# Optimization experiments

Measured on AMD Instinct MI355X. Metric: run time of the kernel, lower is better.

Reference implementation:

```python
import jax, jax.numpy as jnp
import numpy as np

NUM_HEADS = 8
HEAD_SIZE = 64
INPUT = 512
OUT = NUM_HEADS * HEAD_SIZE
B, S = 4, 2048


def setup_inputs() -> dict:
    key = jax.random.key(0)
    ks = jax.random.split(key, 6)
    return {
        "key": jax.random.normal(ks[0], (B, S, INPUT), dtype=jnp.float32),
        "key_mask": jnp.zeros((B, 1, 1, S), dtype=jnp.float32),
        "query": jax.random.normal(ks[1], (B, S, INPUT), dtype=jnp.float32),
        "value": jax.random.normal(ks[2], (B, S, INPUT), dtype=jnp.float32),
        "wq": jax.random.normal(ks[3], (INPUT, OUT), dtype=jnp.float32) * (INPUT ** -0.5),
        "wk": jax.random.normal(ks[4], (INPUT, OUT), dtype=jnp.float32) * (INPUT ** -0.5),
        "wv": jax.random.normal(ks[5], (INPUT, OUT), dtype=jnp.float32) * (INPUT ** -0.5),
    }


def _split_heads(x):
    # [B, S, H*hd] -> [B, H, S, hd]
    b, s, _ = x.shape
    return x.reshape(b, s, NUM_HEADS, HEAD_SIZE).transpose(0, 2, 1, 3)


def reference(key, key_mask, query, value, wq, wk, wv):
    q = _split_heads(query @ wq)   # [B,H,S,hd]
    k = _split_heads(key @ wk)
    v = _split_heads(value @ wv)
    scale = 1.0 / jnp.sqrt(jnp.asarray(HEAD_SIZE, q.dtype))
    logits = jnp.einsum('bhqd,bhkd->bhqk', q, k) * scale + key_mask
    attn = jax.nn.softmax(logits, axis=-1)
    out = jnp.einsum('bhqk,bhkd->bhqd', attn, v)  # [B,H,S,hd]
    out = out.transpose(0, 2, 1, 3).reshape(out.shape[0], out.shape[2], OUT)
    return out
```

## Files before the change

kernel.cpp:

```cpp
#include <hip/hip_runtime.h>

typedef _Float16 f16;
typedef f16 f16x8 __attribute__((ext_vector_type(8)));
typedef f16 f16x4 __attribute__((ext_vector_type(4)));
typedef f16 f16x2 __attribute__((ext_vector_type(2)));
typedef float f32x4 __attribute__((ext_vector_type(4)));
typedef unsigned int u32;

#define MFMA16(a, b, c) __builtin_amdgcn_mfma_f32_16x16x32_f16(a, b, c, 0, 0, 0)

#define BATCH 4
#define NHEADS 8
#define HDIM 64
#define SEQ 2048
#define DIN 512
#define DOUT 512
#define LOG2E 1.44269504f
#define C1 0.18033688f

__device__ __forceinline__ void gl_lds16(const void* g, const void* l) {
  __builtin_amdgcn_global_load_lds(
      (const __attribute__((address_space(1))) u32*)g,
      (__attribute__((address_space(3))) u32*)l, 16, 0, 0);
}

__device__ __forceinline__ float fexp2(float x) {
  float r;
  asm("v_exp_f32 %0, %1" : "=v"(r) : "v"(x));
  return r;
}

__device__ __forceinline__ f16x2 pk2(float a, float b) {
  return __builtin_bit_cast(f16x2, __builtin_amdgcn_cvt_pkrtz(a, b));
}

__device__ __forceinline__ f16x4 pk4(float a, float b, float c, float d) {
  f16x2 u0 = pk2(a, b), u1 = pk2(c, d);
  f16x4 r;
  r[0] = u0[0]; r[1] = u0[1]; r[2] = u1[0]; r[3] = u1[1];
  return r;
}

__global__ __launch_bounds__(256) void prep_w(
    const float* __restrict__ wq, const float* __restrict__ wk,
    const float* __restrict__ wv, f16* __restrict__ wT) {
  __shared__ float tile[64][65];
  const float* w = blockIdx.z == 0 ? wq : (blockIdx.z == 1 ? wk : wv);
  f16* out = wT + (size_t)blockIdx.z * DIN * DOUT;
  int k0 = blockIdx.x * 64, n0 = blockIdx.y * 64;
  int t = threadIdx.x;
  int c = t & 63, rb = t >> 6;
#pragma unroll
  for (int ph = 0; ph < 16; ++ph) {
    int r = ph * 4 + rb;
    tile[r][c] = w[(size_t)(k0 + r) * DOUT + n0 + c];
  }
  __syncthreads();
#pragma unroll
  for (int ph = 0; ph < 16; ++ph) {
    int n = ph * 4 + rb;
    out[(size_t)(n0 + n) * DIN + k0 + c] = (f16)tile[c][n];
  }
}

__global__ __launch_bounds__(256, 3) void qkv_gemm(
    const float* __restrict__ xq, const float* __restrict__ xk,
    const float* __restrict__ xv, const f16* __restrict__ wT,
    f16* __restrict__ Qo, f16* __restrict__ Ko, f16* __restrict__ Vt) {
  __shared__ __attribute__((aligned(16))) f16 smem[16384];
  f16* As = smem;
  f16* Bs = smem + 8192;
  f16* CT = smem;

  int gemm = blockIdx.z;
  const float* x = gemm == 0 ? xq : (gemm == 1 ? xk : xv);
  const f16* wt = wT + (size_t)gemm * DIN * DOUT;
  int bx = blockIdx.x;
  int m0 = (bx & 63) * 128, n0 = (bx >> 6) * 128;
  int t = threadIdx.x, w = t >> 6, lane = t & 63;
  int lr = lane & 15, lq = lane >> 4;
  int wm = (w >> 1) * 64, wn = (w & 1) * 64;

  int tr = t >> 4, tc = t & 15;
  const float* xg = x + (size_t)(m0 + tr) * DIN + tc * 4;
  int aw[8];
#pragma unroll
  for (int ph = 0; ph < 8; ++ph) {
    int r = tr + 16 * ph;
    int phys = (tc >> 1) ^ (r & 7);
    aw[ph] = r * 64 + phys * 8 + (tc & 1) * 4;
  }

  int srow = lane >> 3;
  int schunk = (lane & 7) ^ srow;
  const f16* gb[4];
  const f16* lbb[4];
#pragma unroll
  for (int j = 0; j < 4; ++j) {
    int br = w * 32 + j * 8;
    gb[j] = wt + (size_t)(n0 + br + srow) * DIN + schunk * 8;
    lbb[j] = &Bs[__builtin_amdgcn_readfirstlane(br * 64)];
  }
  int xo0 = ((0 * 4 + lq) ^ (lr & 7)) * 8;
  int xo1 = ((1 * 4 + lq) ^ (lr & 7)) * 8;

  f32x4 zero = {0.f, 0.f, 0.f, 0.f};
  f32x4 acc[4][4];
#pragma unroll
  for (int i = 0; i < 4; ++i)
#pragma unroll
    for (int j = 0; j < 4; ++j) acc[i][j] = zero;

  for (int k0 = 0; k0 < DIN; k0 += 64) {
    __syncthreads();
#pragma unroll
    for (int j = 0; j < 4; ++j) gl_lds16(gb[j] + k0, lbb[j]);
#pragma unroll
    for (int ph = 0; ph < 8; ++ph) {
      float4 a = *(const float4*)(xg + (size_t)ph * 16 * DIN + k0);
      *(f16x4*)&As[aw[ph]] = pk4(a.x, a.y, a.z, a.w);
    }
    __syncthreads();
#pragma unroll
    for (int c = 0; c < 2; ++c) {
      int xo = c ? xo1 : xo0;
      f16x8 xf[4], wf[4];
#pragma unroll
      for (int i = 0; i < 4; ++i)
        xf[i] = *(const f16x8*)&As[(wm + i * 16 + lr) * 64 + xo];
#pragma unroll
      for (int i = 0; i < 4; ++i)
        wf[i] = *(const f16x8*)&Bs[(wn + i * 16 + lr) * 64 + xo];
      if (gemm == 2) {
#pragma unroll
        for (int i = 0; i < 4; ++i)
#pragma unroll
          for (int j = 0; j < 4; ++j)
            acc[i][j] = MFMA16(xf[i], wf[j], acc[i][j]);
      } else {
#pragma unroll
        for (int i = 0; i < 4; ++i)
#pragma unroll
          for (int j = 0; j < 4; ++j)
            acc[i][j] = MFMA16(wf[i], xf[j], acc[i][j]);
      }
    }
  }

  __syncthreads();
  int b_ = m0 >> 11;
  int sl = m0 & 2047;

  if (gemm == 2) {
#pragma unroll
    for (int i = 0; i < 4; ++i) {
#pragma unroll
      for (int j = 0; j < 4; ++j) {
        int d = wn + j * 16 + lr;
        int lc = (wm >> 3) + i * 2 + (lq >> 1);
        int phys = lc ^ lr;
        *(f16x4*)&CT[d * 128 + phys * 8 + (lq & 1) * 4] =
            pk4(acc[i][j][0], acc[i][j][1], acc[i][j][2], acc[i][j][3]);
      }
    }
    __syncthreads();
    int tid16 = t & 15;
#pragma unroll
    for (int ph = 0; ph < 8; ++ph) {
      int d = ph * 16 + (t >> 4);
      int phys = tid16 ^ (d & 15);
      f16x8 vv = *(const f16x8*)&CT[d * 128 + phys * 8];
      int hgl = (n0 + d) >> 6, dd = (n0 + d) & 63;
      *(f16x8*)&Vt[(((size_t)b_ * NHEADS + hgl) * HDIM + dd) * SEQ + sl +
                   tid16 * 8] = vv;
    }
  } else {
    f16* O = gemm == 0 ? Qo : Ko;
    float sc = gemm == 0 ? C1 : 1.0f;
#pragma unroll
    for (int i = 0; i < 4; ++i) {
#pragma unroll
      for (int j = 0; j < 4; ++j) {
        int s = wm + j * 16 + lr;
        int lc = (wn >> 3) + i * 2 + (lq >> 1);
        int phys = lc ^ lr;
        *(f16x4*)&CT[s * 128 + phys * 8 + (lq & 1) * 4] =
            pk4(acc[i][j][0] * sc, acc[i][j][1] * sc, acc[i][j][2] * sc,
                acc[i][j][3] * sc);
      }
    }
    __syncthreads();
    int tid8 = t & 7;
    int hh = (t >> 3) & 1;
#pragma unroll
    for (int ph = 0; ph < 8; ++ph) {
      int s = ph * 16 + (t >> 4);
      int lc = hh * 8 + tid8;
      int phys = lc ^ (s & 15);
      f16x8 vv = *(const f16x8*)&CT[s * 128 + phys * 8];
      int hgl = (n0 >> 6) + hh;
      *(f16x8*)&O[(((size_t)b_ * NHEADS + hgl) * SEQ + sl + s) * HDIM +
                  tid8 * 8] = vv;
    }
  }
}

__global__ __launch_bounds__(256, 3) void flash_attn(
    const f16* __restrict__ Q, const f16* __restrict__ K,
    const f16* __restrict__ Vt, const float* __restrict__ mask,
    float* __restrict__ out) {
  __shared__ __attribute__((aligned(16))) f16 Ks[2][64 * 64];
  __shared__ __attribute__((aligned(16))) f16 Vs[2][64 * 64];
  __shared__ __attribute__((aligned(16))) f16 Ps[128 * 64];

  int bh = blockIdx.x, q0 = blockIdx.y * 128;
  int b = bh >> 3, h = bh & 7;
  int t = threadIdx.x, w = t >> 6, lane = t & 63;
  int lr = lane & 15, lq = lane >> 4;

  const f16* Qg = Q + (size_t)bh * SEQ * HDIM;
  const f16* Kg = K + (size_t)bh * SEQ * HDIM;
  const f16* Vg = Vt + (size_t)bh * HDIM * SEQ;
  const float* mg = mask + (size_t)b * SEQ;

  f16x8 qf[2][2];
#pragma unroll
  for (int u = 0; u < 2; ++u)
#pragma unroll
    for (int c = 0; c < 2; ++c)
      qf[u][c] = *(const f16x8*)(Qg +
                                 (size_t)(q0 + w * 32 + u * 16 + lr) * HDIM +
                                 c * 32 + lq * 8);

  int srow = lane >> 3;
  int sch = (lane & 7) ^ srow;
  const f16* gk0 = Kg + (size_t)(w * 16 + srow) * HDIM + sch * 8;
  const f16* gv0 = Vg + (size_t)(w * 16 + srow) * SEQ + sch * 8;
  int lofs = __builtin_amdgcn_readfirstlane(w * 1024);
  int xk0 = ((0 * 4 + lq) ^ (lr & 7)) * 8;
  int xk1 = ((1 * 4 + lq) ^ (lr & 7)) * 8;

  f32x4 zero = {0.f, 0.f, 0.f, 0.f};
  f32x4 acc[2][4];
#pragma unroll
  for (int u = 0; u < 2; ++u)
#pragma unroll
    for (int i = 0; i < 4; ++i) acc[u][i] = zero;
  float lsum[2] = {0.f, 0.f};

#pragma unroll
  for (int j = 0; j < 2; ++j) {
    gl_lds16(gk0 + (size_t)j * 8 * HDIM, &Ks[0][lofs + j * 512]);
    gl_lds16(gv0 + (size_t)j * 8 * SEQ, &Vs[0][lofs + j * 512]);
  }

  for (int it = 0; it < 32; ++it) {
    int cur = it & 1;
    int k0 = it * 64;
    __syncthreads();
    if (it < 31) {
      int k1 = k0 + 64;
#pragma unroll
      for (int j = 0; j < 2; ++j) {
        gl_lds16(gk0 + (size_t)(k1 + j * 8) * HDIM,
                 &Ks[cur ^ 1][lofs + j * 512]);
        gl_lds16(gv0 + (size_t)j * 8 * SEQ + k1,
                 &Vs[cur ^ 1][lofs + j * 512]);
      }
    }

    f32x4 s[2][4];
#pragma unroll
    for (int nt = 0; nt < 4; ++nt) {
      f16x8 kf0 = *(const f16x8*)&Ks[cur][(nt * 16 + lr) * 64 + xk0];
      f16x8 kf1 = *(const f16x8*)&Ks[cur][(nt * 16 + lr) * 64 + xk1];
      s[0][nt] = MFMA16(kf0, qf[0][0], zero);
      s[0][nt] = MFMA16(kf1, qf[0][1], s[0][nt]);
      s[1][nt] = MFMA16(kf0, qf[1][0], zero);
      s[1][nt] = MFMA16(kf1, qf[1][1], s[1][nt]);
    }

#pragma unroll
    for (int nt = 0; nt < 4; ++nt) {
      float4 mk = *(const float4*)(mg + k0 + nt * 16 + lq * 4);
#pragma unroll
      for (int u = 0; u < 2; ++u) {
        float p0 = fexp2(fmaf(mk.x, LOG2E, s[u][nt][0]));
        float p1 = fexp2(fmaf(mk.y, LOG2E, s[u][nt][1]));
        float p2 = fexp2(fmaf(mk.z, LOG2E, s[u][nt][2]));
        float p3 = fexp2(fmaf(mk.w, LOG2E, s[u][nt][3]));
        lsum[u] += (p0 + p1) + (p2 + p3);
        int phys = (nt * 2 + (lq >> 1)) ^ (lr & 7);
        *(f16x4*)&Ps[(w * 32 + u * 16 + lr) * 64 + phys * 8 + (lq & 1) * 4] =
            pk4(p0, p1, p2, p3);
      }
    }

#pragma unroll
    for (int ks = 0; ks < 2; ++ks) {
      int pc = ((ks * 4 + lq) ^ (lr & 7)) * 8;
      f16x8 ap0 = *(const f16x8*)&Ps[(w * 32 + lr) * 64 + pc];
      f16x8 ap1 = *(const f16x8*)&Ps[(w * 32 + 16 + lr) * 64 + pc];
#pragma unroll
      for (int dt = 0; dt < 4; ++dt) {
        f16x8 bv = *(const f16x8*)&Vs[cur][(dt * 16 + lr) * 64 + pc];
        acc[0][dt] = MFMA16(ap0, bv, acc[0][dt]);
        acc[1][dt] = MFMA16(ap1, bv, acc[1][dt]);
      }
    }
  }

#pragma unroll
  for (int u = 0; u < 2; ++u) {
    float l = lsum[u];
    l += __shfl_xor(l, 16);
    l += __shfl_xor(l, 32);
    float inv = 1.f / l;
    float iv[4];
#pragma unroll
    for (int r = 0; r < 4; ++r) iv[r] = __shfl(inv, lq * 4 + r);
#pragma unroll
    for (int dt = 0; dt < 4; ++dt) {
#pragma unroll
      for (int r = 0; r < 4; ++r) {
        int q = q0 + w * 32 + u * 16 + lq * 4 + r;
        int d = h * HDIM + dt * 16 + lr;
        out[((size_t)b * SEQ + q) * DOUT + d] = acc[u][dt][r] * iv[r];
      }
    }
  }
}

extern "C" void kernel_launch(void* const* d_in, const int* in_sizes, int n_in,
                              void* d_out, int out_size, void* d_ws,
                              size_t ws_size, hipStream_t stream) {
  const float* key = (const float*)d_in[0];
  const float* key_mask = (const float*)d_in[1];
  const float* query = (const float*)d_in[2];
  const float* value = (const float*)d_in[3];
  const float* wq = (const float*)d_in[4];
  const float* wk = (const float*)d_in[5];
  const float* wv = (const float*)d_in[6];
  float* out = (float*)d_out;

  char* ws = (char*)d_ws;
  f16* Qws = (f16*)(ws);
  f16* Kws = (f16*)(ws + 8388608);
  f16* Vtws = (f16*)(ws + 16777216);
  f16* wT = (f16*)(ws + 25165824);

  prep_w<<<dim3(8, 8, 3), 256, 0, stream>>>(wq, wk, wv, wT);
  qkv_gemm<<<dim3(256, 1, 3), 256, 0, stream>>>(query, key, value, wT, Qws,
                                                Kws, Vtws);
  flash_attn<<<dim3(32, 16), 256, 0, stream>>>(Qws, Kws, Vtws, key_mask, out);
}
```

Before: 195.6 us.

## Split attention over key halves with combine kernel, single-buffer K/V

Splits the key sequence into two halves across a new grid z dimension, so twice as many attention blocks run. Each writes unnormalised partial outputs and row sums, and a new combine kernel adds the halves and normalises. The K/V LDS buffers drop from double to single buffering with an extra barrier, and launch bounds move to 4 blocks per CU. The intent is better CU occupancy. In exchange it loses the load/compute overlap and adds extra full-size fp32 output traffic plus a kernel launch.

```diff
diff --git a/kernel.cpp b/kernel.cpp
--- a/kernel.cpp
+++ b/kernel.cpp
@@ -205,15 +205,17 @@
   }
 }
 
-__global__ __launch_bounds__(256, 3) void flash_attn(
+__global__ __launch_bounds__(256, 4) void flash_attn(
     const f16* __restrict__ Q, const f16* __restrict__ K,
     const f16* __restrict__ Vt, const float* __restrict__ mask,
-    float* __restrict__ out) {
-  __shared__ __attribute__((aligned(16))) f16 Ks[2][64 * 64];
-  __shared__ __attribute__((aligned(16))) f16 Vs[2][64 * 64];
+    float* __restrict__ o0, float* __restrict__ o1,
+    float* __restrict__ lpart) {
+  __shared__ __attribute__((aligned(16))) f16 Ks[64 * 64];
+  __shared__ __attribute__((aligned(16))) f16 Vs[64 * 64];
   __shared__ __attribute__((aligned(16))) f16 Ps[128 * 64];
 
-  int bh = blockIdx.x, q0 = blockIdx.y * 128;
+  int bh = blockIdx.x, q0 = blockIdx.y * 128, z = blockIdx.z;
+  int koff = z * 1024;
   int b = bh >> 3, h = bh & 7;
   int t = threadIdx.x, w = t >> 6, lane = t & 63;
   int lr = lane & 15, lq = lane >> 4;
@@ -221,7 +223,7 @@
   const f16* Qg = Q + (size_t)bh * SEQ * HDIM;
   const f16* Kg = K + (size_t)bh * SEQ * HDIM;
   const f16* Vg = Vt + (size_t)bh * HDIM * SEQ;
-  const float* mg = mask + (size_t)b * SEQ;
+  const float* mg = mask + (size_t)b * SEQ + koff;
 
   f16x8 qf[2][2];
 #pragma unroll
@@ -234,8 +236,8 @@
 
   int srow = lane >> 3;
   int sch = (lane & 7) ^ srow;
-  const f16* gk0 = Kg + (size_t)(w * 16 + srow) * HDIM + sch * 8;
-  const f16* gv0 = Vg + (size_t)(w * 16 + srow) * SEQ + sch * 8;
+  const f16* gk0 = Kg + (size_t)(koff + w * 16 + srow) * HDIM + sch * 8;
+  const f16* gv0 = Vg + (size_t)(w * 16 + srow) * SEQ + koff + sch * 8;
   int lofs = __builtin_amdgcn_readfirstlane(w * 1024);
   int xk0 = ((0 * 4 + lq) ^ (lr & 7)) * 8;
   int xk1 = ((1 * 4 + lq) ^ (lr & 7)) * 8;
@@ -248,32 +250,21 @@
     for (int i = 0; i < 4; ++i) acc[u][i] = zero;
   float lsum[2] = {0.f, 0.f};
 
-#pragma unroll
-  for (int j = 0; j < 2; ++j) {
-    gl_lds16(gk0 + (size_t)j * 8 * HDIM, &Ks[0][lofs + j * 512]);
-    gl_lds16(gv0 + (size_t)j * 8 * SEQ, &Vs[0][lofs + j * 512]);
-  }
-
-  for (int it = 0; it < 32; ++it) {
-    int cur = it & 1;
+  for (int it = 0; it < 16; ++it) {
     int k0 = it * 64;
     __syncthreads();
-    if (it < 31) {
-      int k1 = k0 + 64;
-#pragma unroll
-      for (int j = 0; j < 2; ++j) {
-        gl_lds16(gk0 + (size_t)(k1 + j * 8) * HDIM,
-                 &Ks[cur ^ 1][lofs + j * 512]);
-        gl_lds16(gv0 + (size_t)j * 8 * SEQ + k1,
-                 &Vs[cur ^ 1][lofs + j * 512]);
-      }
-    }
+#pragma unroll
+    for (int j = 0; j < 2; ++j) {
+      gl_lds16(gk0 + (size_t)(k0 + j * 8) * HDIM, &Ks[lofs + j * 512]);
+      gl_lds16(gv0 + (size_t)j * 8 * SEQ + k0, &Vs[lofs + j * 512]);
+    }
+    __syncthreads();
 
     f32x4 s[2][4];
 #pragma unroll
     for (int nt = 0; nt < 4; ++nt) {
-      f16x8 kf0 = *(const f16x8*)&Ks[cur][(nt * 16 + lr) * 64 + xk0];
-      f16x8 kf1 = *(const f16x8*)&Ks[cur][(nt * 16 + lr) * 64 + xk1];
+      f16x8 kf0 = *(const f16x8*)&Ks[(nt * 16 + lr) * 64 + xk0];
+      f16x8 kf1 = *(const f16x8*)&Ks[(nt * 16 + lr) * 64 + xk1];
       s[0][nt] = MFMA16(kf0, qf[0][0], zero);
       s[0][nt] = MFMA16(kf1, qf[0][1], s[0][nt]);
       s[1][nt] = MFMA16(kf0, qf[1][0], zero);
@@ -303,32 +294,54 @@
       f16x8 ap1 = *(const f16x8*)&Ps[(w * 32 + 16 + lr) * 64 + pc];
 #pragma unroll
       for (int dt = 0; dt < 4; ++dt) {
-        f16x8 bv = *(const f16x8*)&Vs[cur][(dt * 16 + lr) * 64 + pc];
+        f16x8 bv = *(const f16x8*)&Vs[(dt * 16 + lr) * 64 + pc];
         acc[0][dt] = MFMA16(ap0, bv, acc[0][dt]);
         acc[1][dt] = MFMA16(ap1, bv, acc[1][dt]);
       }
     }
   }
 
+  float* Ob = z == 0 ? o0 : o1;
 #pragma unroll
   for (int u = 0; u < 2; ++u) {
     float l = lsum[u];
     l += __shfl_xor(l, 16);
     l += __shfl_xor(l, 32);
-    float inv = 1.f / l;
-    float iv[4];
-#pragma unroll
-    for (int r = 0; r < 4; ++r) iv[r] = __shfl(inv, lq * 4 + r);
+    if (lq == 0)
+      lpart[z * (32 * SEQ) + bh * SEQ + q0 + w * 32 + u * 16 + lr] = l;
 #pragma unroll
     for (int dt = 0; dt < 4; ++dt) {
 #pragma unroll
       for (int r = 0; r < 4; ++r) {
         int q = q0 + w * 32 + u * 16 + lq * 4 + r;
         int d = h * HDIM + dt * 16 + lr;
-        out[((size_t)b * SEQ + q) * DOUT + d] = acc[u][dt][r] * iv[r];
-      }
-    }
-  }
+        Ob[((size_t)b * SEQ + q) * DOUT + d] = acc[u][dt][r];
+      }
+    }
+  }
+}
+
+__global__ __launch_bounds__(256) void combine(
+    float* __restrict__ o0, const float* __restrict__ o1,
+    const float* __restrict__ lpart) {
+  size_t e = ((size_t)blockIdx.x * 256 + threadIdx.x) * 8;
+  int b = (int)(e >> 20);
+  int s = (int)(e >> 9) & 2047;
+  int h = ((int)e & 511) >> 6;
+  int bh = b * NHEADS + h;
+  float l = lpart[bh * SEQ + s] + lpart[32 * SEQ + bh * SEQ + s];
+  float inv = 1.f / l;
+  float4 a0 = *(const float4*)(o0 + e);
+  float4 a1 = *(const float4*)(o0 + e + 4);
+  float4 c0 = *(const float4*)(o1 + e);
+  float4 c1 = *(const float4*)(o1 + e + 4);
+  float4 r0, r1;
+  r0.x = (a0.x + c0.x) * inv; r0.y = (a0.y + c0.y) * inv;
+  r0.z = (a0.z + c0.z) * inv; r0.w = (a0.w + c0.w) * inv;
+  r1.x = (a1.x + c1.x) * inv; r1.y = (a1.y + c1.y) * inv;
+  r1.z = (a1.z + c1.z) * inv; r1.w = (a1.w + c1.w) * inv;
+  *(float4*)(o0 + e) = r0;
+  *(float4*)(o0 + e + 4) = r1;
 }
 
 extern "C" void kernel_launch(void* const* d_in, const int* in_sizes, int n_in,
@@ -348,9 +361,13 @@
   f16* Kws = (f16*)(ws + 8388608);
   f16* Vtws = (f16*)(ws + 16777216);
   f16* wT = (f16*)(ws + 25165824);
+  float* Opart1 = (float*)(ws + 26738688);
+  float* lpart = (float*)(ws + 43515904);
 
   prep_w<<<dim3(8, 8, 3), 256, 0, stream>>>(wq, wk, wv, wT);
   qkv_gemm<<<dim3(256, 1, 3), 256, 0, stream>>>(query, key, value, wT, Qws,
                                                 Kws, Vtws);
-  flash_attn<<<dim3(32, 16), 256, 0, stream>>>(Qws, Kws, Vtws, key_mask, out);
-}
+  flash_attn<<<dim3(32, 16, 2), 256, 0, stream>>>(Qws, Kws, Vtws, key_mask,
+                                                  out, Opart1, lpart);
+  combine<<<dim3(2048), 256, 0, stream>>>(out, Opart1, lpart);
+}
```

After: 194.0 us. About the same (-0.8%).
